# Optimization experiments

Measured on AMD Instinct MI355X. Metric: run time of the kernel, lower is better.

Reference implementation:

```python
import jax, jax.numpy as jnp
import numpy as np
import math

D_MODEL, N_HEADS, DK, DV, D_FF, GROUP_KV, GW = 1024, 16, 64, 64, 4096, 4, 16
EPS = 1e-6

def _rms(x, w):
    # RMSNorm over last dim: x * rsqrt(mean(x^2)+eps) * weight
    return x * jax.lax.rsqrt(jnp.mean(x * x, axis=-1, keepdims=True) + EPS) * w

def setup_inputs() -> dict:
    key = jax.random.key(0)
    ks = jax.random.split(key, 12)
    s = lambda k, shape, scale: (jax.random.normal(k, shape, dtype=jnp.float32) * scale)
    return {
        "x": s(ks[0], (2, 2048, D_MODEL), 1.0),
        "norm_in_w": jnp.ones((D_MODEL,), jnp.float32),
        "gw": s(ks[1], (GW, D_MODEL), 0.02),
        "Wq": s(ks[2], (D_MODEL, N_HEADS * DK), 1.0 / math.sqrt(D_MODEL)),
        "Wk": s(ks[3], (D_MODEL, GROUP_KV * DK), 1.0 / math.sqrt(D_MODEL)),
        "Wv": s(ks[4], (D_MODEL, GROUP_KV * DV), 1.0 / math.sqrt(D_MODEL)),
        "Wo": s(ks[5], (N_HEADS * DV, D_MODEL), 1.0 / math.sqrt(N_HEADS * DV)),
        "head_norm_w": jnp.ones((N_HEADS, DV), jnp.float32),
        "ff_norm_w": jnp.ones((D_MODEL,), jnp.float32),
        "W1": s(ks[6], (D_MODEL, D_FF), 1.0 / math.sqrt(D_MODEL)),
        "W3": s(ks[7], (D_MODEL, D_FF), 1.0 / math.sqrt(D_MODEL)),
        "W2": s(ks[8], (D_FF, D_MODEL), 1.0 / math.sqrt(D_FF)),
    }

def reference(x, norm_in_w, gw, Wq, Wk, Wv, Wo, head_norm_w, ff_norm_w, W1, W3, W2):
    b, seq, d = x.shape
    R = N_HEADS // GROUP_KV  # heads per kv group
    h = _rms(x, norm_in_w)
    # prepend global workspace tokens
    h = jnp.concatenate([jnp.broadcast_to(gw[None], (b, GW, d)), h], axis=1)
    t = h.shape[1]
    q = (h @ Wq).reshape(b, t, N_HEADS, DK)
    k = jnp.repeat((h @ Wk).reshape(b, t, GROUP_KV, DK), R, axis=2)  # [b,t,H,dk]
    v = jnp.repeat((h @ Wv).reshape(b, t, GROUP_KV, DV), R, axis=2)  # [b,t,H,dv]
    scores = jnp.einsum("bqhd,bkhd->bhqk", q, k) / math.sqrt(DK)
    causal = jnp.arange(t)[:, None] >= jnp.arange(t)[None, :]
    scores = jnp.where(causal[None, None], scores, -jnp.inf)
    weights = jax.nn.softmax(scores, axis=-1)
    ctx = jnp.einsum("bhqk,bkhd->bqhd", weights, v)  # [b,t,H,dv]
    # headwise RMSNorm over dv with per-head weight
    ctx = ctx * jax.lax.rsqrt(jnp.mean(ctx * ctx, axis=-1, keepdims=True) + EPS)
    ctx = ctx * head_norm_w[None, None]
    ctx = ctx.reshape(b, t, N_HEADS * DV)[:, GW:]  # drop gw token outputs
    y = x + ctx @ Wo
    z = _rms(y, ff_norm_w)
    y = y + (jax.nn.silu(z @ W1) * (z @ W3)) @ W2
    return y
```

## Files before the change

kernel.cpp:

```cpp
#include <hip/hip_runtime.h>

typedef unsigned short u16;
typedef __attribute__((ext_vector_type(8))) _Float16 f16x8;
typedef __attribute__((ext_vector_type(4))) float f32x4;

#define TPB 2064
#define NROW 4128
#define VTS 2080

__device__ __forceinline__ u16 f2h(float f) {
    _Float16 h = (_Float16)f;
    return __builtin_bit_cast(u16, h);
}
__device__ __forceinline__ float h2f(u16 u) {
    return (float)__builtin_bit_cast(_Float16, u);
}
__device__ __forceinline__ float wave_sum(float v) {
    #pragma unroll
    for (int m = 32; m; m >>= 1) v += __shfl_xor(v, m, 64);
    return v;
}
__device__ __forceinline__ void gl_lds16(const u16* g, u16* l) {
    __builtin_amdgcn_global_load_lds((const __attribute__((address_space(1))) void*)g,
                                     (__attribute__((address_space(3))) void*)l, 16, 0, 0);
}

__global__ __launch_bounds__(256) void wconv4_kernel(const float* __restrict__ Wq,
                                                     const float* __restrict__ Wk,
                                                     const float* __restrict__ Wv,
                                                     const float* __restrict__ Wo,
                                                     u16* __restrict__ wqkv,
                                                     u16* __restrict__ wo_t) {
    const int z = blockIdx.z;
    const int N = (z == 1 || z == 2) ? 256 : 1024;
    const int n0 = blockIdx.x * 32;
    if (n0 >= N) return;
    const float* src = (z == 0) ? Wq : (z == 1) ? Wk : (z == 2) ? Wv : Wo;
    u16* dst = (z == 0) ? wqkv : (z == 1) ? (wqkv + 1024 * 1024)
             : (z == 2) ? (wqkv + 1280 * 1024) : wo_t;
    __shared__ float tile[32][33];
    const int k0 = blockIdx.y * 32;
    const int tx = threadIdx.x & 31, ty0 = threadIdx.x >> 5;
    #pragma unroll
    for (int r = 0; r < 4; r++) {
        int ky = ty0 + r * 8;
        tile[ky][tx] = src[(size_t)(k0 + ky) * N + n0 + tx];
    }
    __syncthreads();
    #pragma unroll
    for (int r = 0; r < 4; r++) {
        int ny = ty0 + r * 8;
        dst[(size_t)(n0 + ny) * 1024 + k0 + tx] = f2h(tile[tx][ny]);
    }
}

__global__ __launch_bounds__(256) void wconv_t_kernel(const float* __restrict__ src,
                                                      u16* __restrict__ dst, int K, int N) {
    __shared__ float tile[32][33];
    const int k0 = blockIdx.y * 32, n0 = blockIdx.x * 32;
    const int tx = threadIdx.x & 31, ty0 = threadIdx.x >> 5;
    #pragma unroll
    for (int r = 0; r < 4; r++) {
        int ky = ty0 + r * 8;
        tile[ky][tx] = src[(size_t)(k0 + ky) * N + n0 + tx];
    }
    __syncthreads();
    #pragma unroll
    for (int r = 0; r < 4; r++) {
        int ny = ty0 + r * 8;
        dst[(size_t)(n0 + ny) * K + k0 + tx] = f2h(tile[tx][ny]);
    }
}

__global__ __launch_bounds__(256) void wconv_pack13_kernel(const float* __restrict__ W1,
                                                           const float* __restrict__ W3,
                                                           u16* __restrict__ dst) {
    __shared__ float t1[32][33];
    __shared__ float t3[32][33];
    const int f0 = blockIdx.x * 32, k0 = blockIdx.y * 32;
    const int tx = threadIdx.x & 31, ty0 = threadIdx.x >> 5;
    #pragma unroll
    for (int r = 0; r < 4; r++) {
        int ky = ty0 + r * 8;
        t1[ky][tx] = W1[(size_t)(k0 + ky) * 4096 + f0 + tx];
        t3[ky][tx] = W3[(size_t)(k0 + ky) * 4096 + f0 + tx];
    }
    __syncthreads();
    #pragma unroll
    for (int r = 0; r < 4; r++) {
        int fy = ty0 + r * 8;
        int f = f0 + fy;
        int p1 = (f >> 4) * 32 + (f & 15);
        dst[(size_t)p1 * 1024 + k0 + tx] = f2h(t1[tx][fy]);
        dst[(size_t)(p1 + 16) * 1024 + k0 + tx] = f2h(t3[tx][fy]);
    }
}

__global__ __launch_bounds__(256) void vtrans_kernel(const u16* __restrict__ qkv,
                                                     u16* __restrict__ vt) {
    __shared__ u16 tile[32][33];
    const int bg = blockIdx.z;
    const int b = bg >> 2, g = bg & 3;
    const int t0 = blockIdx.x * 32, d0 = blockIdx.y * 32;
    const int tx = threadIdx.x & 31, ty0 = threadIdx.x >> 5;
    #pragma unroll
    for (int r = 0; r < 4; r++) {
        int t = t0 + ty0 + r * 8;
        u16 v = 0;
        if (t < TPB) v = qkv[(size_t)(b * TPB + t) * 1536 + 1280 + g * 64 + d0 + tx];
        tile[ty0 + r * 8][tx] = v;
    }
    __syncthreads();
    #pragma unroll
    for (int r = 0; r < 4; r++) {
        int d = d0 + ty0 + r * 8;
        vt[((size_t)bg * 64 + d) * VTS + t0 + tx] = tile[tx][ty0 + r * 8];
    }
}

__global__ __launch_bounds__(256) void rms_in_kernel(const float* __restrict__ x,
                                                     const float* __restrict__ w,
                                                     const float* __restrict__ gwp,
                                                     u16* __restrict__ h) {
    const int r = blockIdx.x;
    const int b = r / TPB, pos = r - b * TPB;
    const int tid = threadIdx.x;
    u16* hr = h + (size_t)r * 1024;
    if (pos < 16) {
        const float* s = gwp + (size_t)pos * 1024;
        for (int c = tid; c < 1024; c += 256) hr[c] = f2h(s[c]);
        return;
    }
    const float* xr = x + ((size_t)b * 2048 + (pos - 16)) * 1024;
    float v[4]; float ss = 0.f;
    #pragma unroll
    for (int i = 0; i < 4; i++) { v[i] = xr[tid + 256 * i]; ss += v[i] * v[i]; }
    ss = wave_sum(ss);
    __shared__ float red[4];
    if ((tid & 63) == 0) red[tid >> 6] = ss;
    __syncthreads();
    float tot = red[0] + red[1] + red[2] + red[3];
    float rn = rsqrtf(tot * (1.f / 1024.f) + 1e-6f);
    #pragma unroll
    for (int i = 0; i < 4; i++) hr[tid + 256 * i] = f2h(v[i] * rn * w[tid + 256 * i]);
}

__global__ __launch_bounds__(256) void rms_row_kernel(const float* __restrict__ in,
                                                      const float* __restrict__ w,
                                                      u16* __restrict__ out) {
    const int r = blockIdx.x;
    const int tid = threadIdx.x;
    const float* xr = in + (size_t)r * 1024;
    float v[4]; float ss = 0.f;
    #pragma unroll
    for (int i = 0; i < 4; i++) { v[i] = xr[tid + 256 * i]; ss += v[i] * v[i]; }
    ss = wave_sum(ss);
    __shared__ float red[4];
    if ((tid & 63) == 0) red[tid >> 6] = ss;
    __syncthreads();
    float tot = red[0] + red[1] + red[2] + red[3];
    float rn = rsqrtf(tot * (1.f / 1024.f) + 1e-6f);
    u16* orow = out + (size_t)r * 1024;
    #pragma unroll
    for (int i = 0; i < 4; i++) orow[tid + 256 * i] = f2h(v[i] * rn * w[tid + 256 * i]);
}

__global__ __launch_bounds__(256) void combine_kernel(float* __restrict__ out,
                                                      const float* __restrict__ part) {
    const size_t i = ((size_t)blockIdx.x * 256 + threadIdx.x) * 4;
    f32x4 a = *(const f32x4*)&out[i];
    const f32x4 b = *(const f32x4*)&part[i];
    a[0] += b[0]; a[1] += b[1]; a[2] += b[2]; a[3] += b[3];
    *(f32x4*)&out[i] = a;
}

__device__ __forceinline__ void stage_tile(const u16* __restrict__ A, const u16* __restrict__ B,
                                           u16* As, u16* Bs, int m0, int n0, int k0,
                                           int M, int K, int tid) {
    const int wb = tid & ~63;
    #pragma unroll
    for (int t = 0; t < 2; t++) {
        int seg = t * 256 + tid;
        int row = seg >> 2, kc = seg & 3;
        int ar = m0 + row; if (ar > M - 1) ar = M - 1;
        gl_lds16(A + (size_t)ar * K + k0 + kc * 8, As + (size_t)(t * 256 + wb) * 8);
        gl_lds16(B + (size_t)(n0 + row) * K + k0 + kc * 8, Bs + (size_t)(t * 256 + wb) * 8);
    }
}

template <int EPI>
__global__ __launch_bounds__(256, 2) void gemm_bt(const u16* __restrict__ A,
                                                  const u16* __restrict__ B,
                                                  void* Cout,
                                                  const void* aux,
                                                  int M, int N, int K, int swzmode,
                                                  int KL, void* Cout2) {
    __shared__ __align__(16) u16 As[2][4096];
    __shared__ __align__(16) u16 Bs[2][4096];
    const int tid = threadIdx.x;
    const int gx = gridDim.x, gy = gridDim.y;
    int bxs, bys;
    if (swzmode == 2) {
        const int bid = blockIdx.y * gx + blockIdx.x;
        const int xc = bid & 7, cid = bid >> 3;
        const int cx = gx >> 3;
        const int stb = cid / (cx << 3);
        const int rem = cid - stb * (cx << 3);
        const int sm = rem / cx, sn = rem - sm * cx;
        bys = stb * 8 + sm;
        bxs = xc * cx + sn;
    } else {
        const int nwg = gx * gy;
        int lid = swzmode ? (blockIdx.x * gy + blockIdx.y) : (blockIdx.y * gx + blockIdx.x);
        const int q = nwg >> 3, rr = nwg & 7;
        const int xc = lid & 7, o = lid >> 3;
        lid = (xc < rr ? xc * (q + 1) : rr * (q + 1) + (xc - rr) * q) + o;
        if (swzmode) { bxs = lid / gy; bys = lid - bxs * gy; }
        else         { bys = lid / gx; bxs = lid - bys * gx; }
    }
    const int m0 = bys * 128, n0 = bxs * 128;
    const int kbase = blockIdx.z * KL;

    const int w = tid >> 6, l = tid & 63;
    const int wr = w >> 1, wc = w & 1, lr = l & 15, lg = l >> 4;
    f32x4 acc[4][4] = {};
    const int NT = KL >> 5;
    stage_tile(A, B, As[0], Bs[0], m0, n0, kbase, M, K, tid);
    for (int t = 0; t < NT; t++) {
        const int p = t & 1;
        __syncthreads();
        if (t + 1 < NT) stage_tile(A, B, As[p ^ 1], Bs[p ^ 1], m0, n0, kbase + (t + 1) * 32, M, K, tid);
        f16x8 af[4], bf[4];
        #pragma unroll
        for (int i = 0; i < 4; i++) {
            af[i] = *(const f16x8*)&As[p][(wr * 64 + i * 16 + lr) * 32 + lg * 8];
            bf[i] = *(const f16x8*)&Bs[p][(wc * 64 + i * 16 + lr) * 32 + lg * 8];
        }
        #pragma unroll
        for (int i = 0; i < 4; i++)
            #pragma unroll
            for (int j = 0; j < 4; j++)
                acc[i][j] = __builtin_amdgcn_mfma_f32_16x16x32_f16(af[i], bf[j], acc[i][j], 0, 0, 0);
    }
    if constexpr (EPI == 3) {
        const int ldc = N >> 1;
        const int ucol0 = ((n0 + wc * 64) >> 1) + lr;
        #pragma unroll
        for (int i = 0; i < 4; i++) {
            const int rowb = m0 + wr * 64 + i * 16 + lg * 4;
            #pragma unroll
            for (int e = 0; e < 4; e++) {
                const int r2 = rowb + e;
                const float a0 = acc[i][0][e], a1 = acc[i][1][e];
                const float b0 = acc[i][2][e], b1 = acc[i][3][e];
                ((u16*)Cout)[(size_t)r2 * ldc + ucol0] = f2h(a0 / (1.f + __expf(-a0)) * a1);
                ((u16*)Cout)[(size_t)r2 * ldc + ucol0 + 16] = f2h(b0 / (1.f + __expf(-b0)) * b1);
            }
        }
    } else if constexpr (EPI == 4) {
        float* dst0 = (float*)Cout2;
        float* dst1 = (float*)Cout;
        const bool z0 = (blockIdx.z == 0);
        #pragma unroll
        for (int i = 0; i < 4; i++) {
            const int rowb = m0 + wr * 64 + i * 16 + lg * 4;
            #pragma unroll
            for (int j = 0; j < 4; j++) {
                const int col = n0 + wc * 64 + j * 16 + lr;
                #pragma unroll
                for (int e = 0; e < 4; e++) {
                    const int r2 = rowb + e;
                    const size_t idx = (size_t)r2 * N + col;
                    const float v = acc[i][j][e];
                    if (z0) dst0[idx] = v;
                    else    dst1[idx] = v + ((const float*)aux)[idx];
                }
            }
        }
    } else {
        #pragma unroll
        for (int i = 0; i < 4; i++) {
            const int rowb = m0 + wr * 64 + i * 16 + lg * 4;
            #pragma unroll
            for (int j = 0; j < 4; j++) {
                const int col = n0 + wc * 64 + j * 16 + lr;
                #pragma unroll
                for (int e = 0; e < 4; e++) {
                    const int r2 = rowb + e;
                    if (r2 < M) {
                        const size_t idx = (size_t)r2 * N + col;
                        const float v = acc[i][j][e];
                        if constexpr (EPI == 0) {
                            ((u16*)Cout)[idx] = f2h(v);
                        } else {
                            ((float*)Cout)[idx] = v + ((const float*)aux)[idx];
                        }
                    }
                }
            }
        }
    }
}

__global__ __launch_bounds__(256) void attn_kernel(const u16* __restrict__ qkv,
                                                   const u16* __restrict__ vt,
                                                   u16* __restrict__ ctxn,
                                                   const float* __restrict__ hnw) {
    __shared__ __align__(16) u16 Ks[2][2048];
    __shared__ __align__(16) u16 Vs[2][2048];
    const int bx = blockIdx.x, g = blockIdx.y, b = blockIdx.z;
    const int tid = threadIdx.x;
    const int w = tid >> 6, l = tid & 63;
    const int lr = l & 15, lg = l >> 4;
    const int h = g * 4 + w;
    const int sig = 8 * (lr >> 2) + (lr & 3);
    const int LASTROW = TPB - 1;
    const u16* vtb = vt + (size_t)(b * 4 + g) * 64 * VTS;
    const u16* kbase = qkv + (size_t)b * TPB * 1536 + 1024 + g * 64;

    const int krow = tid >> 3;
    const int ksrc = (tid & 7) ^ ((krow & 3) | (((krow >> 3) & 1) << 2));
    const int vdv = tid >> 2;
    const int vsrc = (tid & 3) ^ ((vdv >> 1) & 3);
    const int wb8 = (tid & ~63) * 8;

    const int swzr = (sig & 3) | (((sig >> 3) & 1) << 2);
    const int ka0  = sig * 64 + ((lg ^ swzr) << 3);
    const int ka0b = sig * 64 + (((lg + 4) ^ swzr) << 3);
    const int ka1  = (sig + 4) * 64 + ((lg ^ swzr) << 3);
    const int ka1b = (sig + 4) * 64 + (((lg + 4) ^ swzr) << 3);
    int kv_off[4];
    #pragma unroll
    for (int dt = 0; dt < 4; dt++) {
        const int dv = dt * 16 + lr;
        kv_off[dt] = dv * 32 + ((lg ^ ((dv >> 1) & 3)) << 3);
    }

    const float hw0 = hnw[h * 64 + 0 * 16 + lr];
    const float hw1 = hnw[h * 64 + 1 * 16 + lr];
    const float hw2 = hnw[h * 64 + 2 * 16 + lr];
    const float hw3 = hnw[h * 64 + 3 * 16 + lr];

    for (int half = 0; half < 2; half++) {
        const int qt = half ? (127 - bx) : bx;
        const int orow0 = qt * 16;
        const int qpos0 = 16 + orow0;
        const int qpos = qpos0 + lr;
        const u16* qbase = qkv + (size_t)(b * TPB + qpos) * 1536 + h * 64;
        const f16x8 qf0 = *(const f16x8*)(qbase + lg * 8);
        const f16x8 qf1 = *(const f16x8*)(qbase + 32 + lg * 8);

        float m = -INFINITY, lsum = 0.f;
        f32x4 oc[4] = {};
        const int NT = ((qpos0 + 15) >> 5) + 1;

        __syncthreads();
        gl_lds16(kbase + (size_t)krow * 1536 + ksrc * 8, Ks[0] + wb8);
        gl_lds16(vtb + (size_t)vdv * VTS + vsrc * 8, Vs[0] + wb8);

        for (int kt = 0; kt < NT; kt++) {
            const int p = kt & 1;
            const int kb = kt * 32;
            __syncthreads();
            if (kt + 1 < NT) {
                const int kb2 = kb + 32;
                int kr = kb2 + krow; if (kr > LASTROW) kr = LASTROW;
                gl_lds16(kbase + (size_t)kr * 1536 + ksrc * 8, Ks[p ^ 1] + wb8);
                gl_lds16(vtb + (size_t)vdv * VTS + kb2 + vsrc * 8, Vs[p ^ 1] + wb8);
            }
            const f16x8 a0  = *(const f16x8*)&Ks[p][ka0];
            const f16x8 a0b = *(const f16x8*)&Ks[p][ka0b];
            const f16x8 a1  = *(const f16x8*)&Ks[p][ka1];
            const f16x8 a1b = *(const f16x8*)&Ks[p][ka1b];
            f16x8 vf[4];
            #pragma unroll
            for (int dt = 0; dt < 4; dt++) vf[dt] = *(const f16x8*)&Vs[p][kv_off[dt]];

            f32x4 st0 = {}, st1 = {};
            st0 = __builtin_amdgcn_mfma_f32_16x16x32_f16(a0,  qf0, st0, 0, 0, 0);
            st0 = __builtin_amdgcn_mfma_f32_16x16x32_f16(a0b, qf1, st0, 0, 0, 0);
            st1 = __builtin_amdgcn_mfma_f32_16x16x32_f16(a1,  qf0, st1, 0, 0, 0);
            st1 = __builtin_amdgcn_mfma_f32_16x16x32_f16(a1b, qf1, st1, 0, 0, 0);

            float sv[8]; float bm = -INFINITY;
            if (kb + 31 <= qpos0) {
                #pragma unroll
                for (int j = 0; j < 4; j++) {
                    sv[j] = st0[j] * 0.125f;
                    sv[4 + j] = st1[j] * 0.125f;
                    bm = fmaxf(bm, fmaxf(sv[j], sv[4 + j]));
                }
            } else {
                #pragma unroll
                for (int j = 0; j < 4; j++) {
                    const int kva = kb + 8 * lg + j;
                    float s0 = st0[j] * 0.125f; if (kva > qpos) s0 = -INFINITY;
                    float s1 = st1[j] * 0.125f; if (kva + 4 > qpos) s1 = -INFINITY;
                    sv[j] = s0; sv[4 + j] = s1;
                    bm = fmaxf(bm, fmaxf(s0, s1));
                }
            }
            bm = fmaxf(bm, __shfl_xor(bm, 16, 64));
            bm = fmaxf(bm, __shfl_xor(bm, 32, 64));
            if (!__all(bm - m <= 8.f)) {
                const float nm = fmaxf(m, bm);
                const float sc = __expf(m - nm);
                m = nm;
                lsum *= sc;
                float scj[4];
                #pragma unroll
                for (int j = 0; j < 4; j++) scj[j] = __shfl(sc, 4 * lg + j, 64);
                #pragma unroll
                for (int dt = 0; dt < 4; dt++)
                    #pragma unroll
                    for (int j = 0; j < 4; j++) oc[dt][j] *= scj[j];
            }
            float ps = 0.f;
            f16x8 pa;
            #pragma unroll
            for (int j = 0; j < 8; j++) {
                float p2 = __expf(sv[j] - m);
                ps += p2;
                pa[j] = (_Float16)p2;
            }
            ps += __shfl_xor(ps, 16, 64); ps += __shfl_xor(ps, 32, 64);
            lsum += ps;
            #pragma unroll
            for (int dt = 0; dt < 4; dt++)
                oc[dt] = __builtin_amdgcn_mfma_f32_16x16x32_f16(pa, vf[dt], oc[dt], 0, 0, 0);
        }
        float lj[4];
        #pragma unroll
        for (int j = 0; j < 4; j++) lj[j] = __shfl(lsum, 4 * lg + j, 64);
        float o[4][4]; float ssq[4] = {0, 0, 0, 0};
        #pragma unroll
        for (int dt = 0; dt < 4; dt++)
            #pragma unroll
            for (int j = 0; j < 4; j++) {
                float v = oc[dt][j] / lj[j];
                o[dt][j] = v; ssq[j] += v * v;
            }
        float rj[4];
        #pragma unroll
        for (int j = 0; j < 4; j++) {
            float s = ssq[j];
            s += __shfl_xor(s, 1, 64); s += __shfl_xor(s, 2, 64);
            s += __shfl_xor(s, 4, 64); s += __shfl_xor(s, 8, 64);
            rj[j] = rsqrtf(s * (1.f / 64.f) + 1e-6f);
        }
        const float hwv[4] = {hw0, hw1, hw2, hw3};
        #pragma unroll
        for (int dt = 0; dt < 4; dt++) {
            #pragma unroll
            for (int j = 0; j < 4; j++) {
                const int orow = orow0 + 4 * lg + j;
                ctxn[(size_t)(b * 2048 + orow) * 1024 + h * 64 + dt * 16 + lr] =
                    f2h(o[dt][j] * rj[j] * hwv[dt]);
            }
        }
    }
}

extern "C" void kernel_launch(void* const* d_in, const int* in_sizes, int n_in,
                              void* d_out, int out_size, void* d_ws, size_t ws_size,
                              hipStream_t stream) {
    const float* x   = (const float*)d_in[0];
    const float* wn  = (const float*)d_in[1];
    const float* gw  = (const float*)d_in[2];
    const float* Wq  = (const float*)d_in[3];
    const float* Wk  = (const float*)d_in[4];
    const float* Wv  = (const float*)d_in[5];
    const float* Wo  = (const float*)d_in[6];
    const float* hnw = (const float*)d_in[7];
    const float* wf  = (const float*)d_in[8];
    const float* W1  = (const float*)d_in[9];
    const float* W3  = (const float*)d_in[10];
    const float* W2  = (const float*)d_in[11];

    char* ws = (char*)d_ws;
    u16*  wqkv = (u16*)(ws + 0);
    u16*  wo_t = (u16*)(ws + 3145728);
    u16*  w13t = (u16*)(ws + 5242880);
    u16*  w2t  = (u16*)(ws + 22020096);
    u16*  hbuf = (u16*)(ws + 30408704);
    u16*  qkvb = (u16*)(ws + 38862848);
    u16*  ctxn = hbuf;
    float* scr = (float*)(ws + 30408704);
    float* yb  = (float*)(ws + 51544064);
    u16*  zb   = (u16*)(ws + 68321280);
    u16*  g1   = (u16*)(ws + 76709888);
    u16*  vt   = (u16*)(ws + 110264320);
    float* outp = (float*)d_out;

    const dim3 blk(256);
    wconv4_kernel<<<dim3(32, 32, 4), blk, 0, stream>>>(Wq, Wk, Wv, Wo, wqkv, wo_t);
    wconv_pack13_kernel<<<dim3(128, 32), blk, 0, stream>>>(W1, W3, w13t);
    wconv_t_kernel<<<dim3(32, 128), blk, 0, stream>>>(W2, w2t, 4096, 1024);

    rms_in_kernel<<<dim3(NROW), blk, 0, stream>>>(x, wn, gw, hbuf);
    gemm_bt<0><<<dim3(12, 33), blk, 0, stream>>>(hbuf, wqkv, qkvb, nullptr, NROW, 1536, 1024, 0, 1024, nullptr);
    vtrans_kernel<<<dim3(65, 2, 8), blk, 0, stream>>>(qkvb, vt);
    attn_kernel<<<dim3(64, 4, 2), blk, 0, stream>>>(qkvb, vt, ctxn, hnw);
    gemm_bt<1><<<dim3(8, 32), blk, 0, stream>>>(ctxn, wo_t, yb, x, 4096, 1024, 1024, 0, 1024, nullptr);
    rms_row_kernel<<<dim3(4096), blk, 0, stream>>>(yb, wf, zb);
    gemm_bt<3><<<dim3(64, 32), blk, 0, stream>>>(zb, w13t, g1, nullptr, 4096, 8192, 1024, 2, 1024, nullptr);
    gemm_bt<4><<<dim3(8, 32, 2), blk, 0, stream>>>(g1, w2t, outp, yb, 4096, 1024, 4096, 0, 2048, scr);
    combine_kernel<<<dim3(4096), blk, 0, stream>>>(outp, scr);
}
```

Before: 315.5 us.

## Double attention KV tile to 64 keys and XOR-swizzle GEMM LDS tiles

The attention kernel now stages 64 keys per K/V tile instead of 32, processing two 32-key sub-blocks per barrier. This halves the number of syncthreads and async load rounds, and causal skipping is done per sub-block. The V-transpose stride and grid are widened to cover the padding needed by the larger tile. Separately, the GEMM staging now XOR-swizzles the k-chunk within each LDS row, with matching read offsets, to reduce LDS bank conflicts. The cost is more LDS per attention block and some extra padded key loads on the diagonal tile.

New measurement: 309.9 us, median of 2. No clear change (-1.8%).

```diff
diff --git a/kernel.cpp b/kernel.cpp
--- a/kernel.cpp
+++ b/kernel.cpp
@@ -6,7 +6,7 @@
 
 #define TPB 2064
 #define NROW 4128
-#define VTS 2080
+#define VTS 2112
 
 __device__ __forceinline__ u16 f2h(float f) {
     _Float16 h = (_Float16)f;
@@ -182,9 +182,10 @@
     for (int t = 0; t < 2; t++) {
         int seg = t * 256 + tid;
         int row = seg >> 2, kc = seg & 3;
+        int kcs = (kc ^ ((row >> 1) & 3)) * 8;
         int ar = m0 + row; if (ar > M - 1) ar = M - 1;
-        gl_lds16(A + (size_t)ar * K + k0 + kc * 8, As + (size_t)(t * 256 + wb) * 8);
-        gl_lds16(B + (size_t)(n0 + row) * K + k0 + kc * 8, Bs + (size_t)(t * 256 + wb) * 8);
+        gl_lds16(A + (size_t)ar * K + k0 + kcs, As + (size_t)(t * 256 + wb) * 8);
+        gl_lds16(B + (size_t)(n0 + row) * K + k0 + kcs, Bs + (size_t)(t * 256 + wb) * 8);
     }
 }
 
@@ -223,6 +224,14 @@
 
     const int w = tid >> 6, l = tid & 63;
     const int wr = w >> 1, wc = w & 1, lr = l & 15, lg = l >> 4;
+    int aoff[4], boff[4];
+    #pragma unroll
+    for (int i = 0; i < 4; i++) {
+        const int ra = wr * 64 + i * 16 + lr;
+        aoff[i] = ra * 32 + ((lg ^ ((ra >> 1) & 3)) << 3);
+        const int rb = wc * 64 + i * 16 + lr;
+        boff[i] = rb * 32 + ((lg ^ ((rb >> 1) & 3)) << 3);
+    }
     f32x4 acc[4][4] = {};
     const int NT = KL >> 5;
     stage_tile(A, B, As[0], Bs[0], m0, n0, kbase, M, K, tid);
@@ -233,8 +242,8 @@
         f16x8 af[4], bf[4];
         #pragma unroll
         for (int i = 0; i < 4; i++) {
-            af[i] = *(const f16x8*)&As[p][(wr * 64 + i * 16 + lr) * 32 + lg * 8];
-            bf[i] = *(const f16x8*)&Bs[p][(wc * 64 + i * 16 + lr) * 32 + lg * 8];
+            af[i] = *(const f16x8*)&As[p][aoff[i]];
+            bf[i] = *(const f16x8*)&Bs[p][boff[i]];
         }
         #pragma unroll
         for (int i = 0; i < 4; i++)
@@ -306,8 +315,8 @@
                                                    const u16* __restrict__ vt,
                                                    u16* __restrict__ ctxn,
                                                    const float* __restrict__ hnw) {
-    __shared__ __align__(16) u16 Ks[2][2048];
-    __shared__ __align__(16) u16 Vs[2][2048];
+    __shared__ __align__(16) u16 Ks[2][4096];
+    __shared__ __align__(16) u16 Vs[2][4096];
     const int bx = blockIdx.x, g = blockIdx.y, b = blockIdx.z;
     const int tid = threadIdx.x;
     const int w = tid >> 6, l = tid & 63;
@@ -318,22 +327,31 @@
     const u16* vtb = vt + (size_t)(b * 4 + g) * 64 * VTS;
     const u16* kbase = qkv + (size_t)b * TPB * 1536 + 1024 + g * 64;
 
-    const int krow = tid >> 3;
-    const int ksrc = (tid & 7) ^ ((krow & 3) | (((krow >> 3) & 1) << 2));
-    const int vdv = tid >> 2;
-    const int vsrc = (tid & 3) ^ ((vdv >> 1) & 3);
     const int wb8 = (tid & ~63) * 8;
-
-    const int swzr = (sig & 3) | (((sig >> 3) & 1) << 2);
-    const int ka0  = sig * 64 + ((lg ^ swzr) << 3);
-    const int ka0b = sig * 64 + (((lg + 4) ^ swzr) << 3);
-    const int ka1  = (sig + 4) * 64 + ((lg ^ swzr) << 3);
-    const int ka1b = (sig + 4) * 64 + (((lg + 4) ^ swzr) << 3);
-    int kv_off[4];
-    #pragma unroll
-    for (int dt = 0; dt < 4; dt++) {
-        const int dv = dt * 16 + lr;
-        kv_off[dt] = dv * 32 + ((lg ^ ((dv >> 1) & 3)) << 3);
+    int srow[2], ksrc[2], vsrc[2];
+    #pragma unroll
+    for (int s = 0; s < 2; s++) {
+        const int slot = s * 256 + tid;
+        const int row = slot >> 3, kc = slot & 7;
+        srow[s] = row;
+        ksrc[s] = (kc ^ ((row + 2 * (row >> 3)) & 7)) * 8;
+        vsrc[s] = (kc ^ (row & 7)) * 8;
+    }
+
+    int ka0[2], ka0b[2], ka1[2], ka1b[2], kvo[2][4];
+    #pragma unroll
+    for (int sub = 0; sub < 2; sub++) {
+        const int r0 = sub * 32 + sig, r1 = r0 + 4;
+        const int s0 = (r0 + 2 * (r0 >> 3)) & 7, s1 = (r1 + 2 * (r1 >> 3)) & 7;
+        ka0[sub]  = r0 * 64 + ((lg ^ s0) << 3);
+        ka0b[sub] = r0 * 64 + (((lg + 4) ^ s0) << 3);
+        ka1[sub]  = r1 * 64 + ((lg ^ s1) << 3);
+        ka1b[sub] = r1 * 64 + (((lg + 4) ^ s1) << 3);
+        #pragma unroll
+        for (int dt = 0; dt < 4; dt++) {
+            const int dv = dt * 16 + lr;
+            kvo[sub][dt] = dv * 64 + (((lg + sub * 4) ^ (dv & 7)) << 3);
+        }
     }
 
     const float hw0 = hnw[h * 64 + 0 * 16 + lr];
@@ -352,82 +370,95 @@
 
         float m = -INFINITY, lsum = 0.f;
         f32x4 oc[4] = {};
-        const int NT = ((qpos0 + 15) >> 5) + 1;
+        const int NT = ((qpos0 + 15) >> 6) + 1;
 
         __syncthreads();
-        gl_lds16(kbase + (size_t)krow * 1536 + ksrc * 8, Ks[0] + wb8);
-        gl_lds16(vtb + (size_t)vdv * VTS + vsrc * 8, Vs[0] + wb8);
+        #pragma unroll
+        for (int s = 0; s < 2; s++) {
+            int kr = srow[s]; if (kr > LASTROW) kr = LASTROW;
+            gl_lds16(kbase + (size_t)kr * 1536 + ksrc[s], Ks[0] + s * 2048 + wb8);
+            gl_lds16(vtb + (size_t)srow[s] * VTS + vsrc[s], Vs[0] + s * 2048 + wb8);
+        }
 
         for (int kt = 0; kt < NT; kt++) {
             const int p = kt & 1;
-            const int kb = kt * 32;
+            const int kb = kt * 64;
             __syncthreads();
             if (kt + 1 < NT) {
-                const int kb2 = kb + 32;
-                int kr = kb2 + krow; if (kr > LASTROW) kr = LASTROW;
-                gl_lds16(kbase + (size_t)kr * 1536 + ksrc * 8, Ks[p ^ 1] + wb8);
-                gl_lds16(vtb + (size_t)vdv * VTS + kb2 + vsrc * 8, Vs[p ^ 1] + wb8);
-            }
-            const f16x8 a0  = *(const f16x8*)&Ks[p][ka0];
-            const f16x8 a0b = *(const f16x8*)&Ks[p][ka0b];
-            const f16x8 a1  = *(const f16x8*)&Ks[p][ka1];
-            const f16x8 a1b = *(const f16x8*)&Ks[p][ka1b];
-            f16x8 vf[4];
-            #pragma unroll
-            for (int dt = 0; dt < 4; dt++) vf[dt] = *(const f16x8*)&Vs[p][kv_off[dt]];
-
-            f32x4 st0 = {}, st1 = {};
-            st0 = __builtin_amdgcn_mfma_f32_16x16x32_f16(a0,  qf0, st0, 0, 0, 0);
-            st0 = __builtin_amdgcn_mfma_f32_16x16x32_f16(a0b, qf1, st0, 0, 0, 0);
-            st1 = __builtin_amdgcn_mfma_f32_16x16x32_f16(a1,  qf0, st1, 0, 0, 0);
-            st1 = __builtin_amdgcn_mfma_f32_16x16x32_f16(a1b, qf1, st1, 0, 0, 0);
-
-            float sv[8]; float bm = -INFINITY;
-            if (kb + 31 <= qpos0) {
+                const int kb2 = kb + 64;
                 #pragma unroll
-                for (int j = 0; j < 4; j++) {
-                    sv[j] = st0[j] * 0.125f;
-                    sv[4 + j] = st1[j] * 0.125f;
-                    bm = fmaxf(bm, fmaxf(sv[j], sv[4 + j]));
+                for (int s = 0; s < 2; s++) {
+                    int kr = kb2 + srow[s]; if (kr > LASTROW) kr = LASTROW;
+                    gl_lds16(kbase + (size_t)kr * 1536 + ksrc[s], Ks[p ^ 1] + s * 2048 + wb8);
+                    gl_lds16(vtb + (size_t)srow[s] * VTS + kb2 + vsrc[s], Vs[p ^ 1] + s * 2048 + wb8);
                 }
-            } else {
-                #pragma unroll
-                for (int j = 0; j < 4; j++) {
-                    const int kva = kb + 8 * lg + j;
-                    float s0 = st0[j] * 0.125f; if (kva > qpos) s0 = -INFINITY;
-                    float s1 = st1[j] * 0.125f; if (kva + 4 > qpos) s1 = -INFINITY;
-                    sv[j] = s0; sv[4 + j] = s1;
-                    bm = fmaxf(bm, fmaxf(s0, s1));
+            }
+            #pragma unroll
+            for (int sub = 0; sub < 2; sub++) {
+                const int kb32 = kb + sub * 32;
+                if (kb32 <= qpos0 + 15) {
+                    const f16x8 a0  = *(const f16x8*)&Ks[p][ka0[sub]];
+                    const f16x8 a0b = *(const f16x8*)&Ks[p][ka0b[sub]];
+                    const f16x8 a1  = *(const f16x8*)&Ks[p][ka1[sub]];
+                    const f16x8 a1b = *(const f16x8*)&Ks[p][ka1b[sub]];
+                    f16x8 vf[4];
+                    #pragma unroll
+                    for (int dt = 0; dt < 4; dt++) vf[dt] = *(const f16x8*)&Vs[p][kvo[sub][dt]];
+
+                    f32x4 st0 = {}, st1 = {};
+                    st0 = __builtin_amdgcn_mfma_f32_16x16x32_f16(a0,  qf0, st0, 0, 0, 0);
+                    st0 = __builtin_amdgcn_mfma_f32_16x16x32_f16(a0b, qf1, st0, 0, 0, 0);
+                    st1 = __builtin_amdgcn_mfma_f32_16x16x32_f16(a1,  qf0, st1, 0, 0, 0);
+                    st1 = __builtin_amdgcn_mfma_f32_16x16x32_f16(a1b, qf1, st1, 0, 0, 0);
+
+                    float sv[8]; float bm = -INFINITY;
+                    if (kb32 + 31 <= qpos0) {
+                        #pragma unroll
+                        for (int j = 0; j < 4; j++) {
+                            sv[j] = st0[j] * 0.125f;
+                            sv[4 + j] = st1[j] * 0.125f;
+                            bm = fmaxf(bm, fmaxf(sv[j], sv[4 + j]));
+                        }
+                    } else {
+                        #pragma unroll
+                        for (int j = 0; j < 4; j++) {
+                            const int kva = kb32 + 8 * lg + j;
+                            float s0 = st0[j] * 0.125f; if (kva > qpos) s0 = -INFINITY;
+                            float s1 = st1[j] * 0.125f; if (kva + 4 > qpos) s1 = -INFINITY;
+                            sv[j] = s0; sv[4 + j] = s1;
+                            bm = fmaxf(bm, fmaxf(s0, s1));
+                        }
+                    }
+                    bm = fmaxf(bm, __shfl_xor(bm, 16, 64));
+                    bm = fmaxf(bm, __shfl_xor(bm, 32, 64));
+                    if (!__all(bm - m <= 8.f)) {
+                        const float nm = fmaxf(m, bm);
+                        const float sc = __expf(m - nm);
+                        m = nm;
+                        lsum *= sc;
+                        float scj[4];
+                        #pragma unroll
+                        for (int j = 0; j < 4; j++) scj[j] = __shfl(sc, 4 * lg + j, 64);
+                        #pragma unroll
+                        for (int dt = 0; dt < 4; dt++)
+                            #pragma unroll
+                            for (int j = 0; j < 4; j++) oc[dt][j] *= scj[j];
+                    }
+                    float ps = 0.f;
+                    f16x8 pa;
+                    #pragma unroll
+                    for (int j = 0; j < 8; j++) {
+                        float p2 = __expf(sv[j] - m);
+                        ps += p2;
+                        pa[j] = (_Float16)p2;
+                    }
+                    ps += __shfl_xor(ps, 16, 64); ps += __shfl_xor(ps, 32, 64);
+                    lsum += ps;
+                    #pragma unroll
+                    for (int dt = 0; dt < 4; dt++)
+                        oc[dt] = __builtin_amdgcn_mfma_f32_16x16x32_f16(pa, vf[dt], oc[dt], 0, 0, 0);
                 }
             }
-            bm = fmaxf(bm, __shfl_xor(bm, 16, 64));
-            bm = fmaxf(bm, __shfl_xor(bm, 32, 64));
-            if (!__all(bm - m <= 8.f)) {
-                const float nm = fmaxf(m, bm);
-                const float sc = __expf(m - nm);
-                m = nm;
-                lsum *= sc;
-                float scj[4];
-                #pragma unroll
-                for (int j = 0; j < 4; j++) scj[j] = __shfl(sc, 4 * lg + j, 64);
-                #pragma unroll
-                for (int dt = 0; dt < 4; dt++)
-                    #pragma unroll
-                    for (int j = 0; j < 4; j++) oc[dt][j] *= scj[j];
-            }
-            float ps = 0.f;
-            f16x8 pa;
-            #pragma unroll
-            for (int j = 0; j < 8; j++) {
-                float p2 = __expf(sv[j] - m);
-                ps += p2;
-                pa[j] = (_Float16)p2;
-            }
-            ps += __shfl_xor(ps, 16, 64); ps += __shfl_xor(ps, 32, 64);
-            lsum += ps;
-            #pragma unroll
-            for (int dt = 0; dt < 4; dt++)
-                oc[dt] = __builtin_amdgcn_mfma_f32_16x16x32_f16(pa, vf[dt], oc[dt], 0, 0, 0);
         }
         float lj[4];
         #pragma unroll
@@ -499,7 +530,7 @@
 
     rms_in_kernel<<<dim3(NROW), blk, 0, stream>>>(x, wn, gw, hbuf);
     gemm_bt<0><<<dim3(12, 33), blk, 0, stream>>>(hbuf, wqkv, qkvb, nullptr, NROW, 1536, 1024, 0, 1024, nullptr);
-    vtrans_kernel<<<dim3(65, 2, 8), blk, 0, stream>>>(qkvb, vt);
+    vtrans_kernel<<<dim3(66, 2, 8), blk, 0, stream>>>(qkvb, vt);
     attn_kernel<<<dim3(64, 4, 2), blk, 0, stream>>>(qkvb, vt, ctxn, hnw);
     gemm_bt<1><<<dim3(8, 32), blk, 0, stream>>>(ctxn, wo_t, yb, x, 4096, 1024, 1024, 0, 1024, nullptr);
     rms_row_kernel<<<dim3(4096), blk, 0, stream>>>(yb, wf, zb);
```
